# Kernel optimization log

Measured on AMD Instinct MI355X. Metric: run time of the kernel, lower is better.

## Reference

```python
import jax, jax.numpy as jnp
import numpy as np

T = 300  # windowsize = windowstep(50) * windowmul(6)
D_IN = 39
H1, H2 = 35, 30
FC1, FC2, OUT = 50, 40, 2


def _lstm_layer(x_tbd, W, b, H):
    """TF LSTMCell: gates ordered i, j, f, o; forget_bias=1.0; tanh activation.
    x_tbd: [T, B, D]; W: [D+H, 4H]; b: [4H]. Returns hidden states [T, B, H]."""
    B = x_tbd.shape[1]
    h0 = jnp.zeros((B, H), x_tbd.dtype)
    c0 = jnp.zeros((B, H), x_tbd.dtype)

    def step(carry, xt):
        h, c = carry
        z = jnp.concatenate([xt, h], axis=-1) @ W + b  # [B, 4H]
        i, j, f, o = jnp.split(z, 4, axis=-1)
        c = jax.nn.sigmoid(f + 1.0) * c + jax.nn.sigmoid(i) * jnp.tanh(j)
        h = jax.nn.sigmoid(o) * jnp.tanh(c)
        return (h, c), h

    _, hs = jax.lax.scan(step, (h0, c0), x_tbd)
    return hs


def _stack(x_tbd, W1, b1, W2, b2):
    h1 = _lstm_layer(x_tbd, W1, b1, H1)
    return _lstm_layer(h1, W2, b2, H2)


def setup_inputs() -> dict:
    key = jax.random.key(0)
    ks = jax.random.split(key, 16)
    B = 4096
    s = lambda fan_in: 1.0 / np.sqrt(fan_in)

    def mat(k, shape):
        return jax.random.normal(k, shape, jnp.float32) * s(shape[0])

    return {
        "x": jax.random.normal(ks[0], (B, T, D_IN), jnp.float32),
        "fw_W1": mat(ks[1], (D_IN + H1, 4 * H1)), "fw_b1": jnp.zeros((4 * H1,), jnp.float32),
        "fw_W2": mat(ks[2], (H1 + H2, 4 * H2)), "fw_b2": jnp.zeros((4 * H2,), jnp.float32),
        "bw_W1": mat(ks[3], (D_IN + H1, 4 * H1)), "bw_b1": jnp.zeros((4 * H1,), jnp.float32),
        "bw_W2": mat(ks[4], (H1 + H2, 4 * H2)), "bw_b2": jnp.zeros((4 * H2,), jnp.float32),
        "W_fc1": mat(ks[5], (2 * H2, FC1)), "b_fc1": jnp.zeros((FC1,), jnp.float32),
        "W_fc2": mat(ks[6], (FC1, FC2)), "b_fc2": jnp.zeros((FC2,), jnp.float32),
        "W_out": mat(ks[7], (FC2, OUT)), "b_out": jnp.zeros((OUT,), jnp.float32),
    }


def reference(x, fw_W1, fw_b1, fw_W2, fw_b2, bw_W1, bw_b1, bw_W2, bw_b2,
              W_fc1, b_fc1, W_fc2, b_fc2, W_out, b_out):
    x_tbd = jnp.transpose(x, (1, 0, 2))  # [T, B, D]
    h_fw = _stack(x_tbd, fw_W1, fw_b1, fw_W2, fw_b2)               # [T, B, H2]
    h_bw = _stack(x_tbd[::-1], bw_W1, bw_b1, bw_W2, bw_b2)[::-1]   # [T, B, H2]
    h = jnp.concatenate([h_fw, h_bw], axis=-1)  # [T, B, 2*H2]
    h = jnp.transpose(h, (1, 0, 2))             # [B, T, 60]
    h = jax.nn.relu(h @ W_fc1 + b_fc1)
    h = jax.nn.relu(h @ W_fc2 + b_fc2)
    logits = h @ W_out + b_out                  # [B, T, 2]
    return logits
```

## Files before the change

kernel.cpp:

```cpp
#include <hip/hip_runtime.h>


#define T_STEPS 300
#define DIN 39
#define H1 35
#define H2 30
#define BATCH 4096
#define FC1N 50
#define FC2N 40

#define AP_STR 104

typedef _Float16 f16;
typedef _Float16 half8 __attribute__((ext_vector_type(8)));
typedef float floatx4 __attribute__((ext_vector_type(4)));

__device__ __forceinline__ float sigf(float x) {
    return __builtin_amdgcn_rcpf(1.0f + __expf(-x));
}
__device__ __forceinline__ float tanh_f(float x) {
    return 1.0f - 2.0f * __builtin_amdgcn_rcpf(1.0f + __expf(2.0f * x));
}

__global__ void wprep_kernel(const float* __restrict__ fw1, const float* __restrict__ bw1,
                             const float* __restrict__ fw2, const float* __restrict__ bw2,
                             f16* __restrict__ bp) {
    int frag = blockIdx.x;
    int lane = threadIdx.x;
    int dir = frag / 60;
    int rem = frag % 60;
    int layer = (rem < 36) ? 0 : 1;
    int r2 = (layer == 0) ? rem : rem - 36;
    int ug = r2 / 12, g = (r2 % 12) / 3, c = r2 % 3;
    int u = ug * 16 + (lane & 15);
    const float* W = (layer == 0) ? (dir ? bw1 : fw1) : (dir ? bw2 : fw2);
    for (int j = 0; j < 8; ++j) {
        int k = c * 32 + (lane >> 4) * 8 + j;
        float v = 0.0f;
        if (layer == 0) {
            if (u < H1) {
                int kr = (k < 39) ? k : ((k >= 40 && k < 75) ? k - 1 : -1);
                if (kr >= 0) v = W[kr * (4 * H1) + g * H1 + u];
            }
        } else {
            if (u < H2 && k < 65) v = W[k * (4 * H2) + g * H2 + u];
        }
        bp[(size_t)frag * 512 + lane * 8 + j] = (f16)v;
    }
}

__global__ void fcwprep_kernel(const float* __restrict__ Wf1, const float* __restrict__ Wf2,
                               const float* __restrict__ Wo, f16* __restrict__ fcp) {
    int f = blockIdx.x;
    int lane = threadIdx.x;
    int lm = lane & 15, oct = lane >> 4;
    for (int j = 0; j < 8; ++j) {
        float v = 0.0f;
        if (f < 8) {
            int tile = f >> 1, chunk = f & 1;
            int n = tile * 16 + lm;
            int kl = chunk * 32 + oct * 8 + j;
            int krow = (kl < 30) ? kl : ((kl >= 32 && kl < 62) ? kl - 2 : -1);
            if (n < FC1N && krow >= 0) v = Wf1[krow * FC1N + n];
        } else if (f < 14) {
            int g = f - 8, tile = g >> 1, chunk = g & 1;
            int n = tile * 16 + lm;
            int k = chunk * 32 + oct * 8 + j;
            if (n < FC2N && k < FC1N) v = Wf2[k * FC2N + n];
        } else {
            int chunk = f - 14;
            int k = chunk * 32 + oct * 8 + j;
            if (lm < 2 && k < FC2N) v = Wo[k * 2 + lm];
        }
        fcp[(size_t)f * 512 + lane * 8 + j] = (f16)v;
    }
}

__global__ __launch_bounds__(192, 2) void lstm_fused(
    const float* __restrict__ x, const f16* __restrict__ bp,
    const float* __restrict__ fb1, const float* __restrict__ bb1,
    const float* __restrict__ fb2, const float* __restrict__ bb2,
    f16* __restrict__ h2s)
{
    __shared__ f16 pan1[2][16 * AP_STR];
    __shared__ f16 pan2[2][16 * AP_STR];

    const int tid = threadIdx.x;
    const int b0  = blockIdx.x * 16;
    const int dir = blockIdx.y;
    const int wv   = tid >> 6;
    const int lane = tid & 63;
    const int lm = lane & 15, oct = lane >> 4;
    const float* b1 = dir ? bb1 : fb1;
    const float* b2 = dir ? bb2 : fb2;
    const int u1 = wv * 16 + lm;

    half8 bf1[4][3], bf2[4][3];
    #pragma unroll
    for (int g = 0; g < 4; ++g)
        #pragma unroll
        for (int c = 0; c < 3; ++c)
            bf1[g][c] = *(const half8*)(bp + (size_t)(dir * 60 + wv * 12 + g * 3 + c) * 512 + lane * 8);
    if (wv < 2) {
        #pragma unroll
        for (int g = 0; g < 4; ++g)
            #pragma unroll
            for (int c = 0; c < 3; ++c)
                bf2[g][c] = *(const half8*)(bp + (size_t)(dir * 60 + 36 + wv * 12 + g * 3 + c) * 512 + lane * 8);
    }

    float zb1[4], zb2[4];
    #pragma unroll
    for (int g = 0; g < 4; ++g) {
        zb1[g] = (u1 < H1) ? b1[g * H1 + u1] : 0.f;
        zb2[g] = (wv < 2 && u1 < H2) ? b2[g * H2 + u1] : 0.f;
    }
    float c1[4] = {0.f, 0.f, 0.f, 0.f};
    float c2[4] = {0.f, 0.f, 0.f, 0.f};

    for (int idx = tid; idx < 16 * AP_STR; idx += 192) {
        pan1[0][idx] = (f16)0.f; pan1[1][idx] = (f16)0.f;
        pan2[0][idx] = (f16)0.f; pan2[1][idx] = (f16)0.f;
    }
    __syncthreads();

    const int sr = tid / 10, sq = tid % 10;
    float xv[4] = {0.f, 0.f, 0.f, 0.f};
    if (tid < 160) {
        int t0 = dir ? (T_STEPS - 1) : 0;
        const float* p0 = x + ((size_t)(b0 + sr) * T_STEPS + t0) * DIN;
        union { f16 h[4]; uint2 u; } pk;
        #pragma unroll
        for (int i = 0; i < 4; ++i) { int k = sq * 4 + i; pk.h[i] = (k < DIN) ? (f16)p0[k] : (f16)0.f; }
        *(uint2*)(&pan1[0][sr * AP_STR + sq * 4]) = pk.u;
        int t1 = dir ? (T_STEPS - 2) : 1;
        const float* p1 = x + ((size_t)(b0 + sr) * T_STEPS + t1) * DIN;
        #pragma unroll
        for (int i = 0; i < 4; ++i) { int k = sq * 4 + i; xv[i] = (k < DIN) ? p1[k] : 0.f; }
    }
    __syncthreads();

    const int arow = lm * AP_STR + oct * 8;

    {
        floatx4 C[4];
        #pragma unroll
        for (int g = 0; g < 4; ++g) C[g] = (floatx4){zb1[g], zb1[g], zb1[g], zb1[g]};
        half8 a0 = *(const half8*)(&pan1[0][arow]);
        half8 a1 = *(const half8*)(&pan1[0][arow + 32]);
        half8 a2 = *(const half8*)(&pan1[0][arow + 64]);
        #pragma unroll
        for (int g = 0; g < 4; ++g) {
            C[g] = __builtin_amdgcn_mfma_f32_16x16x32_f16(a0, bf1[g][0], C[g], 0, 0, 0);
            C[g] = __builtin_amdgcn_mfma_f32_16x16x32_f16(a1, bf1[g][1], C[g], 0, 0, 0);
            C[g] = __builtin_amdgcn_mfma_f32_16x16x32_f16(a2, bf1[g][2], C[g], 0, 0, 0);
        }
        #pragma unroll
        for (int r = 0; r < 4; ++r) {
            float cc = sigf(C[2][r] + 1.0f) * c1[r] + sigf(C[0][r]) * tanh_f(C[1][r]);
            c1[r] = cc;
            float hh = sigf(C[3][r]) * tanh_f(cc);
            if (u1 < H1) {
                int row = oct * 4 + r;
                f16 hv = (f16)hh;
                pan1[1][row * AP_STR + 40 + u1] = hv;
                pan2[1][row * AP_STR + u1] = hv;
            }
        }
    }
    if (tid < 160) {
        union { f16 h[4]; uint2 u; } pk;
        #pragma unroll
        for (int i = 0; i < 4; ++i) pk.h[i] = (f16)xv[i];
        *(uint2*)(&pan1[1][sr * AP_STR + sq * 4]) = pk.u;
        int t2 = dir ? (T_STEPS - 3) : 2;
        const float* p2 = x + ((size_t)(b0 + sr) * T_STEPS + t2) * DIN;
        #pragma unroll
        for (int i = 0; i < 4; ++i) { int k = sq * 4 + i; xv[i] = (k < DIN) ? p2[k] : 0.f; }
    }
    __syncthreads();

    for (int s = 0; s < T_STEPS; ++s) {
        const int p = 1 - (s & 1);

        float xn[4] = {0.f, 0.f, 0.f, 0.f};
        if (tid < 160) {
            int sp = s + 3; if (sp > T_STEPS - 1) sp = T_STEPS - 1;
            int tp = dir ? (T_STEPS - 1 - sp) : sp;
            const float* px = x + ((size_t)(b0 + sr) * T_STEPS + tp) * DIN;
            #pragma unroll
            for (int i = 0; i < 4; ++i) { int k = sq * 4 + i; xn[i] = (k < DIN) ? px[k] : 0.f; }
        }

        floatx4 C1g[4], C2g[4];
        #pragma unroll
        for (int g = 0; g < 4; ++g) C1g[g] = (floatx4){zb1[g], zb1[g], zb1[g], zb1[g]};
        {
            half8 a0 = *(const half8*)(&pan1[p][arow]);
            half8 a1 = *(const half8*)(&pan1[p][arow + 32]);
            half8 a2 = *(const half8*)(&pan1[p][arow + 64]);
            #pragma unroll
            for (int g = 0; g < 4; ++g) {
                C1g[g] = __builtin_amdgcn_mfma_f32_16x16x32_f16(a0, bf1[g][0], C1g[g], 0, 0, 0);
                C1g[g] = __builtin_amdgcn_mfma_f32_16x16x32_f16(a1, bf1[g][1], C1g[g], 0, 0, 0);
                C1g[g] = __builtin_amdgcn_mfma_f32_16x16x32_f16(a2, bf1[g][2], C1g[g], 0, 0, 0);
            }
        }
        if (wv < 2) {
            #pragma unroll
            for (int g = 0; g < 4; ++g) C2g[g] = (floatx4){zb2[g], zb2[g], zb2[g], zb2[g]};
            half8 a0 = *(const half8*)(&pan2[p][arow]);
            half8 a1 = *(const half8*)(&pan2[p][arow + 32]);
            half8 a2 = *(const half8*)(&pan2[p][arow + 64]);
            #pragma unroll
            for (int g = 0; g < 4; ++g) {
                C2g[g] = __builtin_amdgcn_mfma_f32_16x16x32_f16(a0, bf2[g][0], C2g[g], 0, 0, 0);
                C2g[g] = __builtin_amdgcn_mfma_f32_16x16x32_f16(a1, bf2[g][1], C2g[g], 0, 0, 0);
                C2g[g] = __builtin_amdgcn_mfma_f32_16x16x32_f16(a2, bf2[g][2], C2g[g], 0, 0, 0);
            }
        }

        f16* w1 = &pan1[1 - p][0];
        f16* w2 = &pan2[1 - p][0];
        #pragma unroll
        for (int r = 0; r < 4; ++r) {
            float cc = sigf(C1g[2][r] + 1.0f) * c1[r] + sigf(C1g[0][r]) * tanh_f(C1g[1][r]);
            c1[r] = cc;
            float hh = sigf(C1g[3][r]) * tanh_f(cc);
            if (u1 < H1) {
                int row = oct * 4 + r;
                f16 hv = (f16)hh;
                w1[row * AP_STR + 40 + u1] = hv;
                w2[row * AP_STR + u1] = hv;
            }
        }
        const int t_out = dir ? (T_STEPS - 1 - s) : s;
        if (wv < 2) {
            #pragma unroll
            for (int r = 0; r < 4; ++r) {
                float dd = sigf(C2g[2][r] + 1.0f) * c2[r] + sigf(C2g[0][r]) * tanh_f(C2g[1][r]);
                c2[r] = dd;
                float gg = sigf(C2g[3][r]) * tanh_f(dd);
                if (u1 < H2) {
                    int row = oct * 4 + r;
                    f16 gv = (f16)gg;
                    w2[row * AP_STR + 35 + u1] = gv;
                    h2s[((size_t)(dir * BATCH + b0 + row) * T_STEPS + t_out) * 32 + u1] = gv;
                }
            }
        }

        if (tid < 160) {
            union { f16 h[4]; uint2 u; } pk;
            #pragma unroll
            for (int i = 0; i < 4; ++i) pk.h[i] = (f16)xv[i];
            *(uint2*)(&pan1[1 - p][sr * AP_STR + sq * 4]) = pk.u;
            #pragma unroll
            for (int i = 0; i < 4; ++i) xv[i] = xn[i];
        }
        __syncthreads();
    }
}

__global__ __launch_bounds__(256) void fc_kernel(
    const f16* __restrict__ h2s, const f16* __restrict__ fcp,
    const float* __restrict__ bf1, const float* __restrict__ bf2,
    const float* __restrict__ bo, float* __restrict__ out)
{
    __shared__ f16 apf[4][16 * 72];
    const int tid = threadIdx.x;
    const int wv = tid >> 6, lane = tid & 63;
    const int lm = lane & 15, oct = lane >> 4;
    f16* ap = apf[wv];

    half8 wf[16];
    #pragma unroll
    for (int f = 0; f < 16; ++f)
        wf[f] = *(const half8*)(fcp + (size_t)f * 512 + lane * 8);

    const int ar = lm * 72 + oct * 8;

    for (int it = 0; it < 4; ++it) {
        const size_t rid0 = (size_t)blockIdx.x * 256 + wv * 64 + it * 16;

        {
            int row = lane >> 2, seg = lane & 3;
            uint4 vf = *(const uint4*)(h2s + (rid0 + row) * 32 + seg * 8);
            uint4 vb = *(const uint4*)(h2s + ((size_t)BATCH * T_STEPS + rid0 + row) * 32 + seg * 8);
            *(uint4*)(ap + row * 72 + seg * 8) = vf;
            *(uint4*)(ap + row * 72 + 32 + seg * 8) = vb;
        }

        {
            half8 a0 = *(const half8*)(ap + ar);
            half8 a1 = *(const half8*)(ap + ar + 32);
            floatx4 C[4];
            #pragma unroll
            for (int t = 0; t < 4; ++t) {
                int col = t * 16 + lm;
                float b = (col < FC1N) ? bf1[col] : 0.f;
                C[t] = (floatx4){b, b, b, b};
                C[t] = __builtin_amdgcn_mfma_f32_16x16x32_f16(a0, wf[t * 2 + 0], C[t], 0, 0, 0);
                C[t] = __builtin_amdgcn_mfma_f32_16x16x32_f16(a1, wf[t * 2 + 1], C[t], 0, 0, 0);
            }
            #pragma unroll
            for (int t = 0; t < 4; ++t) {
                int col = t * 16 + lm;
                #pragma unroll
                for (int r = 0; r < 4; ++r)
                    ap[(oct * 4 + r) * 72 + col] = (f16)fmaxf(C[t][r], 0.f);
            }
        }
        {
            half8 a0 = *(const half8*)(ap + ar);
            half8 a1 = *(const half8*)(ap + ar + 32);
            floatx4 D[3];
            #pragma unroll
            for (int t = 0; t < 3; ++t) {
                int col = t * 16 + lm;
                float b = (col < FC2N) ? bf2[col] : 0.f;
                D[t] = (floatx4){b, b, b, b};
                D[t] = __builtin_amdgcn_mfma_f32_16x16x32_f16(a0, wf[8 + t * 2 + 0], D[t], 0, 0, 0);
                D[t] = __builtin_amdgcn_mfma_f32_16x16x32_f16(a1, wf[8 + t * 2 + 1], D[t], 0, 0, 0);
            }
            #pragma unroll
            for (int t = 0; t < 3; ++t) {
                int col = t * 16 + lm;
                #pragma unroll
                for (int r = 0; r < 4; ++r)
                    ap[(oct * 4 + r) * 72 + col] = (f16)fmaxf(D[t][r], 0.f);
            }
        }
        {
            half8 a0 = *(const half8*)(ap + ar);
            half8 a1 = *(const half8*)(ap + ar + 32);
            float b = (lm < 2) ? bo[lm] : 0.f;
            floatx4 E = (floatx4){b, b, b, b};
            E = __builtin_amdgcn_mfma_f32_16x16x32_f16(a0, wf[14], E, 0, 0, 0);
            E = __builtin_amdgcn_mfma_f32_16x16x32_f16(a1, wf[15], E, 0, 0, 0);
            if (lm < 2) {
                #pragma unroll
                for (int r = 0; r < 4; ++r)
                    out[(rid0 + oct * 4 + r) * 2 + lm] = E[r];
            }
        }
    }
}

extern "C" void kernel_launch(void* const* d_in, const int* in_sizes, int n_in,
                              void* d_out, int out_size, void* d_ws, size_t ws_size,
                              hipStream_t stream) {
    const float* x     = (const float*)d_in[0];
    const float* fw_W1 = (const float*)d_in[1];
    const float* fw_b1 = (const float*)d_in[2];
    const float* fw_W2 = (const float*)d_in[3];
    const float* fw_b2 = (const float*)d_in[4];
    const float* bw_W1 = (const float*)d_in[5];
    const float* bw_b1 = (const float*)d_in[6];
    const float* bw_W2 = (const float*)d_in[7];
    const float* bw_b2 = (const float*)d_in[8];
    const float* Wf1   = (const float*)d_in[9];
    const float* bf1   = (const float*)d_in[10];
    const float* Wf2   = (const float*)d_in[11];
    const float* bf2   = (const float*)d_in[12];
    const float* Wo    = (const float*)d_in[13];
    const float* bo    = (const float*)d_in[14];
    float* outp = (float*)d_out;

    f16* h2s = (f16*)d_ws;
    f16* bp  = h2s + (size_t)2 * BATCH * T_STEPS * 32;
    f16* fcp = bp + (size_t)120 * 512;

    wprep_kernel<<<120, 64, 0, stream>>>(fw_W1, bw_W1, fw_W2, bw_W2, bp);
    fcwprep_kernel<<<16, 64, 0, stream>>>(Wf1, Wf2, Wo, fcp);

    dim3 gl(BATCH / 16, 2);
    lstm_fused<<<gl, 192, 0, stream>>>(x, bp, fw_b1, bw_b1, fw_b2, bw_b2, h2s);

    fc_kernel<<<(BATCH * T_STEPS) / 256, 256, 0, stream>>>(
        h2s, fcp, bf1, bf2, bo, outp);
}
```

Before: 803.1 us.

## Split LSTM layer-2 work onto dedicated waves, 320-thread blocks

Layer-2 gate computation moves off waves 0-1, which used to do both layers each step, onto two extra waves (wv 3,4). Each wave now holds one set of B fragments and one cell state, and runs one layer per step, so the per-step critical path and register pressure both shrink. The cost is more threads per block (320 instead of 192) and a launch bound asking for 3 blocks per CU, which may limit occupancy or make the per-step barrier more expensive.

```diff
diff --git a/kernel.cpp b/kernel.cpp
--- a/kernel.cpp
+++ b/kernel.cpp
@@ -76,7 +76,7 @@
     }
 }
 
-__global__ __launch_bounds__(192, 2) void lstm_fused(
+__global__ __launch_bounds__(320, 3) void lstm_fused(
     const float* __restrict__ x, const f16* __restrict__ bp,
     const float* __restrict__ fb1, const float* __restrict__ bb1,
     const float* __restrict__ fb2, const float* __restrict__ bb2,
@@ -91,34 +91,27 @@
     const int wv   = tid >> 6;
     const int lane = tid & 63;
     const int lm = lane & 15, oct = lane >> 4;
-    const float* b1 = dir ? bb1 : fb1;
-    const float* b2 = dir ? bb2 : fb2;
-    const int u1 = wv * 16 + lm;
-
-    half8 bf1[4][3], bf2[4][3];
+    const bool isL2 = (wv >= 3);
+    const int ug = isL2 ? (wv - 3) : wv;
+    const int u  = ug * 16 + lm;
+    const int Hn = isL2 ? H2 : H1;
+    const float* bias = isL2 ? (dir ? bb2 : fb2) : (dir ? bb1 : fb1);
+    const int fragbase = dir * 60 + (isL2 ? 36 : 0) + ug * 12;
+
+    half8 bf[4][3];
     #pragma unroll
     for (int g = 0; g < 4; ++g)
         #pragma unroll
         for (int c = 0; c < 3; ++c)
-            bf1[g][c] = *(const half8*)(bp + (size_t)(dir * 60 + wv * 12 + g * 3 + c) * 512 + lane * 8);
-    if (wv < 2) {
-        #pragma unroll
-        for (int g = 0; g < 4; ++g)
-            #pragma unroll
-            for (int c = 0; c < 3; ++c)
-                bf2[g][c] = *(const half8*)(bp + (size_t)(dir * 60 + 36 + wv * 12 + g * 3 + c) * 512 + lane * 8);
-    }
-
-    float zb1[4], zb2[4];
+            bf[g][c] = *(const half8*)(bp + (size_t)(fragbase + g * 3 + c) * 512 + lane * 8);
+
+    float zb[4];
     #pragma unroll
-    for (int g = 0; g < 4; ++g) {
-        zb1[g] = (u1 < H1) ? b1[g * H1 + u1] : 0.f;
-        zb2[g] = (wv < 2 && u1 < H2) ? b2[g * H2 + u1] : 0.f;
-    }
-    float c1[4] = {0.f, 0.f, 0.f, 0.f};
-    float c2[4] = {0.f, 0.f, 0.f, 0.f};
-
-    for (int idx = tid; idx < 16 * AP_STR; idx += 192) {
+    for (int g = 0; g < 4; ++g)
+        zb[g] = (u < Hn) ? bias[g * Hn + u] : 0.f;
+    float cst[4] = {0.f, 0.f, 0.f, 0.f};
+
+    for (int idx = tid; idx < 16 * AP_STR; idx += 320) {
         pan1[0][idx] = (f16)0.f; pan1[1][idx] = (f16)0.f;
         pan2[0][idx] = (f16)0.f; pan2[1][idx] = (f16)0.f;
     }
@@ -142,29 +135,29 @@
 
     const int arow = lm * AP_STR + oct * 8;
 
-    {
+    if (!isL2) {
         floatx4 C[4];
         #pragma unroll
-        for (int g = 0; g < 4; ++g) C[g] = (floatx4){zb1[g], zb1[g], zb1[g], zb1[g]};
+        for (int g = 0; g < 4; ++g) C[g] = (floatx4){zb[g], zb[g], zb[g], zb[g]};
         half8 a0 = *(const half8*)(&pan1[0][arow]);
         half8 a1 = *(const half8*)(&pan1[0][arow + 32]);
         half8 a2 = *(const half8*)(&pan1[0][arow + 64]);
         #pragma unroll
         for (int g = 0; g < 4; ++g) {
-            C[g] = __builtin_amdgcn_mfma_f32_16x16x32_f16(a0, bf1[g][0], C[g], 0, 0, 0);
-            C[g] = __builtin_amdgcn_mfma_f32_16x16x32_f16(a1, bf1[g][1], C[g], 0, 0, 0);
-            C[g] = __builtin_amdgcn_mfma_f32_16x16x32_f16(a2, bf1[g][2], C[g], 0, 0, 0);
+            C[g] = __builtin_amdgcn_mfma_f32_16x16x32_f16(a0, bf[g][0], C[g], 0, 0, 0);
+            C[g] = __builtin_amdgcn_mfma_f32_16x16x32_f16(a1, bf[g][1], C[g], 0, 0, 0);
+            C[g] = __builtin_amdgcn_mfma_f32_16x16x32_f16(a2, bf[g][2], C[g], 0, 0, 0);
         }
         #pragma unroll
         for (int r = 0; r < 4; ++r) {
-            float cc = sigf(C[2][r] + 1.0f) * c1[r] + sigf(C[0][r]) * tanh_f(C[1][r]);
-            c1[r] = cc;
+            float cc = sigf(C[2][r] + 1.0f) * cst[r] + sigf(C[0][r]) * tanh_f(C[1][r]);
+            cst[r] = cc;
             float hh = sigf(C[3][r]) * tanh_f(cc);
-            if (u1 < H1) {
+            if (u < H1) {
                 int row = oct * 4 + r;
                 f16 hv = (f16)hh;
-                pan1[1][row * AP_STR + 40 + u1] = hv;
-                pan2[1][row * AP_STR + u1] = hv;
+                pan1[1][row * AP_STR + 40 + u] = hv;
+                pan2[1][row * AP_STR + u] = hv;
             }
         }
     }
@@ -192,60 +185,49 @@
             for (int i = 0; i < 4; ++i) { int k = sq * 4 + i; xn[i] = (k < DIN) ? px[k] : 0.f; }
         }
 
-        floatx4 C1g[4], C2g[4];
-        #pragma unroll
-        for (int g = 0; g < 4; ++g) C1g[g] = (floatx4){zb1[g], zb1[g], zb1[g], zb1[g]};
-        {
-            half8 a0 = *(const half8*)(&pan1[p][arow]);
-            half8 a1 = *(const half8*)(&pan1[p][arow + 32]);
-            half8 a2 = *(const half8*)(&pan1[p][arow + 64]);
+        const f16* ap = isL2 ? &pan2[p][0] : &pan1[p][0];
+        floatx4 C[4];
+        #pragma unroll
+        for (int g = 0; g < 4; ++g) C[g] = (floatx4){zb[g], zb[g], zb[g], zb[g]};
+        {
+            half8 a0 = *(const half8*)(ap + arow);
+            half8 a1 = *(const half8*)(ap + arow + 32);
+            half8 a2 = *(const half8*)(ap + arow + 64);
             #pragma unroll
             for (int g = 0; g < 4; ++g) {
-                C1g[g] = __builtin_amdgcn_mfma_f32_16x16x32_f16(a0, bf1[g][0], C1g[g], 0, 0, 0);
-                C1g[g] = __builtin_amdgcn_mfma_f32_16x16x32_f16(a1, bf1[g][1], C1g[g], 0, 0, 0);
-                C1g[g] = __builtin_amdgcn_mfma_f32_16x16x32_f16(a2, bf1[g][2], C1g[g], 0, 0, 0);
-            }
-        }
-        if (wv < 2) {
-            #pragma unroll
-            for (int g = 0; g < 4; ++g) C2g[g] = (floatx4){zb2[g], zb2[g], zb2[g], zb2[g]};
-            half8 a0 = *(const half8*)(&pan2[p][arow]);
-            half8 a1 = *(const half8*)(&pan2[p][arow + 32]);
-            half8 a2 = *(const half8*)(&pan2[p][arow + 64]);
-            #pragma unroll
-            for (int g = 0; g < 4; ++g) {
-                C2g[g] = __builtin_amdgcn_mfma_f32_16x16x32_f16(a0, bf2[g][0], C2g[g], 0, 0, 0);
-                C2g[g] = __builtin_amdgcn_mfma_f32_16x16x32_f16(a1, bf2[g][1], C2g[g], 0, 0, 0);
-                C2g[g] = __builtin_amdgcn_mfma_f32_16x16x32_f16(a2, bf2[g][2], C2g[g], 0, 0, 0);
+                C[g] = __builtin_amdgcn_mfma_f32_16x16x32_f16(a0, bf[g][0], C[g], 0, 0, 0);
+                C[g] = __builtin_amdgcn_mfma_f32_16x16x32_f16(a1, bf[g][1], C[g], 0, 0, 0);
+                C[g] = __builtin_amdgcn_mfma_f32_16x16x32_f16(a2, bf[g][2], C[g], 0, 0, 0);
             }
         }
 
         f16* w1 = &pan1[1 - p][0];
         f16* w2 = &pan2[1 - p][0];
-        #pragma unroll
-        for (int r = 0; r < 4; ++r) {
-            float cc = sigf(C1g[2][r] + 1.0f) * c1[r] + sigf(C1g[0][r]) * tanh_f(C1g[1][r]);
-            c1[r] = cc;
-            float hh = sigf(C1g[3][r]) * tanh_f(cc);
-            if (u1 < H1) {
-                int row = oct * 4 + r;
-                f16 hv = (f16)hh;
-                w1[row * AP_STR + 40 + u1] = hv;
-                w2[row * AP_STR + u1] = hv;
-            }
-        }
-        const int t_out = dir ? (T_STEPS - 1 - s) : s;
-        if (wv < 2) {
+        if (!isL2) {
             #pragma unroll
             for (int r = 0; r < 4; ++r) {
-                float dd = sigf(C2g[2][r] + 1.0f) * c2[r] + sigf(C2g[0][r]) * tanh_f(C2g[1][r]);
-                c2[r] = dd;
-                float gg = sigf(C2g[3][r]) * tanh_f(dd);
-                if (u1 < H2) {
+                float cc = sigf(C[2][r] + 1.0f) * cst[r] + sigf(C[0][r]) * tanh_f(C[1][r]);
+                cst[r] = cc;
+                float hh = sigf(C[3][r]) * tanh_f(cc);
+                if (u < H1) {
+                    int row = oct * 4 + r;
+                    f16 hv = (f16)hh;
+                    w1[row * AP_STR + 40 + u] = hv;
+                    w2[row * AP_STR + u] = hv;
+                }
+            }
+        } else {
+            const int t_out = dir ? (T_STEPS - 1 - s) : s;
+            #pragma unroll
+            for (int r = 0; r < 4; ++r) {
+                float dd = sigf(C[2][r] + 1.0f) * cst[r] + sigf(C[0][r]) * tanh_f(C[1][r]);
+                cst[r] = dd;
+                float gg = sigf(C[3][r]) * tanh_f(dd);
+                if (u < H2) {
                     int row = oct * 4 + r;
                     f16 gv = (f16)gg;
-                    w2[row * AP_STR + 35 + u1] = gv;
-                    h2s[((size_t)(dir * BATCH + b0 + row) * T_STEPS + t_out) * 32 + u1] = gv;
+                    w2[row * AP_STR + 35 + u] = gv;
+                    h2s[((size_t)(dir * BATCH + b0 + row) * T_STEPS + t_out) * 32 + u] = gv;
                 }
             }
         }
@@ -375,7 +357,7 @@
     fcwprep_kernel<<<16, 64, 0, stream>>>(Wf1, Wf2, Wo, fcp);
 
     dim3 gl(BATCH / 16, 2);
-    lstm_fused<<<gl, 192, 0, stream>>>(x, bp, fw_b1, bw_b1, fw_b2, bw_b2, h2s);
+    lstm_fused<<<gl, 320, 0, stream>>>(x, bp, fw_b1, bw_b1, fw_b2, bw_b2, h2s);
 
     fc_kernel<<<(BATCH * T_STEPS) / 256, 256, 0, stream>>>(
         h2s, fcp, bf1, bf2, bo, outp);
```

Result: faster. 698.7 us (-13.0%).
